# Kernel tuning notes

Measured on AMD Instinct MI355X. Metric: run time of the kernel, lower is better.

The kernel has to match this reference:

```python
import jax, jax.numpy as jnp
import numpy as np

EPS = 1e-3  # BatchNormalization epsilon


def setup_inputs() -> dict:
    key = jax.random.key(0)
    ks = jax.random.split(key, 8)
    B, H, W, C = 16, 128, 128, 128
    f = C // 2  # filters = max(1, C // 2)
    x = jax.random.normal(ks[0], (B, H, W, C), dtype=jnp.float32)
    s_in = 1.0 / np.sqrt(C)
    s_f = 1.0 / np.sqrt(f)
    return {
        "x": x,
        "Wg": jax.random.normal(ks[1], (C, f), dtype=jnp.float32) * s_in,
        "bg": jnp.zeros((f,), jnp.float32),
        "Wt": jax.random.normal(ks[2], (C, f), dtype=jnp.float32) * s_in,
        "bt": jnp.zeros((f,), jnp.float32),
        "Wp": jax.random.normal(ks[3], (C, f), dtype=jnp.float32) * s_in,
        "bp": jnp.zeros((f,), jnp.float32),
        "Wo": jax.random.normal(ks[4], (f, f), dtype=jnp.float32) * s_f,
        "bo": jnp.zeros((f,), jnp.float32),
        "gamma": jnp.ones((f,), jnp.float32),
        "beta": jnp.zeros((f,), jnp.float32),
        "moving_mean": jnp.zeros((f,), jnp.float32),
        "moving_var": jnp.ones((f,), jnp.float32),
    }


def reference(x, Wg, bg, Wt, bt, Wp, bp, Wo, bo, gamma, beta, moving_mean, moving_var):
    B, H, W, C = x.shape
    f = Wg.shape[1]
    N = H * W
    # 1x1 conv projections (NHWC): einsum over channel dim, then flatten spatial
    g = (jnp.einsum('bhwc,cf->bhwf', x, Wg) + bg).reshape(B, N, f)     # [B,N,f]
    tx = (jnp.einsum('bhwc,cf->bhwf', x, Wt) + bt).reshape(B, N, f)    # theta
    ty = (jnp.einsum('bhwc,cf->bhwf', x, Wp) + bp).reshape(B, N, f)    # phi
    # keras Dot(axes=[1,2]) on ([B,N,f], Permute->[B,f,N]) contracts the N axes
    # -> f x f Gram matrix per batch element.
    fm = jnp.einsum('bni,bnj->bij', tx, ty)                            # [B,f,f]
    fm = jax.nn.softmax(fm, axis=-1)
    # second Dot(axes=[1,2]): contract fm axis 1 (i) with g axis 2 (i) -> [B,f,N]
    z = jnp.einsum('bij,bni->bjn', fm, g)                              # [B,f,N]
    # Reshape flat-reinterprets [B, f*N] as [B,H,W,f]
    z = z.reshape(B, H, W, f)
    # output 1x1 conv (f -> f channels)
    z = jnp.einsum('bhwf,fe->bhwe', z, Wo) + bo
    # BatchNorm, inference mode (moving statistics)
    inv = gamma * jax.lax.rsqrt(moving_var + EPS)
    z = (z - moving_mean) * inv + beta
    return z
```

## Files before the change

kernel.cpp:

```cpp
#include <hip/hip_runtime.h>
#include <stdint.h>

#define B_ 16
#define H_ 128
#define W_ 128
#define C_ 128
#define F_ 64
#define N_ (H_*W_)
#define SPLITS 32
#define RPB (N_/SPLITS)
#define CH 64
#define NCH (RPB/CH)
#define EPSV 1e-3f

typedef __attribute__((ext_vector_type(8))) short bf16x8;
typedef __attribute__((ext_vector_type(16))) float f32x16;

__device__ __forceinline__ unsigned short f2b(float f) {
    unsigned int x = __float_as_uint(f);
    x += 0x7fffu + ((x >> 16) & 1u);
    return (unsigned short)(x >> 16);
}
__device__ __forceinline__ float b2f(unsigned short u) {
    return __uint_as_float(((unsigned int)u) << 16);
}

__global__ __launch_bounds__(256, 2)
void kS(const float* __restrict__ x, const float* __restrict__ Wg,
        const float* __restrict__ bg, unsigned short* __restrict__ g,
        float* __restrict__ Spart, float* __restrict__ cspart)
{
    __shared__ unsigned int  xsT_hi[C_][36];
    __shared__ unsigned int  xsT_lo[C_][36];
    __shared__ __align__(16) unsigned short xs_pool[CH][136];
    __shared__ __align__(16) unsigned short gT[CH][72];

    const int tid  = threadIdx.x;
    const int lane = tid & 63;
    const int w    = tid >> 6;
    const int b    = blockIdx.x >> 5;
    const int sp   = blockIdx.x & 31;

    const float* xb = x + ((size_t)b * N_ + (size_t)sp * RPB) * C_;
    unsigned short* gb = g + ((size_t)b * N_ + (size_t)sp * RPB) * F_;

    const int rowA = lane & 31;
    const int hiL  = lane >> 5;
    const int kgrp = hiL * 8;
    const int c1b  = (w & 1) * 64;
    const int c2b  = (w >> 1) * 64;
    const int nbG  = (w & 1) * 32;
    const int fbG  = (w >> 1) * 32;

    const float bgl = bg[fbG + rowA];

    for (int i = tid; i < C_*F_; i += 256) {
        int c = i >> 6, f = i & 63;
        xs_pool[f][c] = f2b(Wg[i]);
    }
    __syncthreads();
    bf16x8 wgfr[8];
    #pragma unroll
    for (int ks = 0; ks < 8; ++ks)
        wgfr[ks] = *(const bf16x8*)&xs_pool[fbG + rowA][ks*16 + kgrp];
    __syncthreads();

    f32x16 accS[2][2];
    #pragma unroll
    for (int ti = 0; ti < 2; ++ti)
        #pragma unroll
        for (int tj = 0; tj < 2; ++tj)
            #pragma unroll
            for (int e = 0; e < 16; ++e) accS[ti][tj][e] = 0.f;

    float4 csr[4];
    #pragma unroll
    for (int p = 0; p < 4; ++p) csr[p] = make_float4(0.f, 0.f, 0.f, 0.f);

    const int sr = tid >> 2;
    const int sc = (tid & 3) * 16;

    for (int ch = 0; ch < NCH; ++ch) {
        __syncthreads();

        float4 ra[4], rq[4];
        {
            const float* xc = xb + (size_t)ch * CH * C_;
            #pragma unroll
            for (int p = 0; p < 4; ++p) {
                const int idx = tid + 256*p;
                const float* r0 = xc + (size_t)(2*(idx & 31)) * C_ + ((idx >> 5) * 4);
                ra[p] = *(const float4*)r0;
                rq[p] = *(const float4*)(r0 + C_);
            }
        }
        uint4 gv0, gv1;
        if (ch) {
            gv0 = *(const uint4*)&gT[sr][sc];
            gv1 = *(const uint4*)&gT[sr][sc + 8];
        }

        #pragma unroll
        for (int p = 0; p < 4; ++p) {
            const int idx = tid + 256*p;
            const int np  = idx & 31;
            const int c4  = (idx >> 5) * 4;
            float4 a = ra[p], q = rq[p];
            csr[p].x += a.x + q.x;
            csr[p].y += a.y + q.y;
            csr[p].z += a.z + q.z;
            csr[p].w += a.w + q.w;
            unsigned short ha0 = f2b(a.x), ha1 = f2b(a.y), ha2 = f2b(a.z), ha3 = f2b(a.w);
            unsigned short hb0 = f2b(q.x), hb1 = f2b(q.y), hb2 = f2b(q.z), hb3 = f2b(q.w);
            unsigned short la0 = f2b(a.x - b2f(ha0)), la1 = f2b(a.y - b2f(ha1));
            unsigned short la2 = f2b(a.z - b2f(ha2)), la3 = f2b(a.w - b2f(ha3));
            unsigned short lb0 = f2b(q.x - b2f(hb0)), lb1 = f2b(q.y - b2f(hb1));
            unsigned short lb2 = f2b(q.z - b2f(hb2)), lb3 = f2b(q.w - b2f(hb3));
            xsT_hi[c4+0][np] = (unsigned)ha0 | ((unsigned)hb0 << 16);
            xsT_hi[c4+1][np] = (unsigned)ha1 | ((unsigned)hb1 << 16);
            xsT_hi[c4+2][np] = (unsigned)ha2 | ((unsigned)hb2 << 16);
            xsT_hi[c4+3][np] = (unsigned)ha3 | ((unsigned)hb3 << 16);
            xsT_lo[c4+0][np] = (unsigned)la0 | ((unsigned)lb0 << 16);
            xsT_lo[c4+1][np] = (unsigned)la1 | ((unsigned)lb1 << 16);
            xsT_lo[c4+2][np] = (unsigned)la2 | ((unsigned)lb2 << 16);
            xsT_lo[c4+3][np] = (unsigned)la3 | ((unsigned)lb3 << 16);
            ushort4 u0; u0.x = ha0; u0.y = ha1; u0.z = ha2; u0.w = ha3;
            ushort4 u1; u1.x = hb0; u1.y = hb1; u1.z = hb2; u1.w = hb3;
            *(ushort4*)&xs_pool[2*np  ][c4] = u0;
            *(ushort4*)&xs_pool[2*np+1][c4] = u1;
        }

        if (ch) {
            unsigned short* dst = gb + (size_t)((ch-1)*CH + sr) * F_ + sc;
            *(uint4*)dst       = gv0;
            *(uint4*)(dst + 8) = gv1;
        }
        __syncthreads();

        {
            f32x16 aG;
            #pragma unroll
            for (int e = 0; e < 16; ++e) aG[e] = 0.f;
            #pragma unroll
            for (int ks = 0; ks < 8; ++ks) {
                bf16x8 av = *(const bf16x8*)&xs_pool[nbG + rowA][ks*16 + kgrp];
                aG = __builtin_amdgcn_mfma_f32_32x32x16_bf16(av, wgfr[ks], aG, 0, 0, 0);
            }
            const int fcol = fbG + rowA;
            #pragma unroll
            for (int r = 0; r < 16; ++r) {
                int nloc = (r & 3) + 8*(r >> 2) + 4*hiL;
                gT[nbG + nloc][fcol] = f2b(aG[r] + bgl);
            }
        }

        #pragma unroll
        for (int ks = 0; ks < 4; ++ks) {
            const int kn = ks*16 + kgrp;
            bf16x8 Ah[2], Al[2], Bh[2], Bl[2];
            #pragma unroll
            for (int t = 0; t < 2; ++t) {
                const unsigned short* rAh = (const unsigned short*)&xsT_hi[c1b + 32*t + rowA][0];
                const unsigned short* rAl = (const unsigned short*)&xsT_lo[c1b + 32*t + rowA][0];
                Ah[t] = *(const bf16x8*)(rAh + kn);
                Al[t] = *(const bf16x8*)(rAl + kn);
                const unsigned short* rBh = (const unsigned short*)&xsT_hi[c2b + 32*t + rowA][0];
                const unsigned short* rBl = (const unsigned short*)&xsT_lo[c2b + 32*t + rowA][0];
                Bh[t] = *(const bf16x8*)(rBh + kn);
                Bl[t] = *(const bf16x8*)(rBl + kn);
            }
            #pragma unroll
            for (int ti = 0; ti < 2; ++ti)
                #pragma unroll
                for (int tj = 0; tj < 2; ++tj) {
                    accS[ti][tj] = __builtin_amdgcn_mfma_f32_32x32x16_bf16(Ah[ti], Bh[tj], accS[ti][tj], 0, 0, 0);
                    accS[ti][tj] = __builtin_amdgcn_mfma_f32_32x32x16_bf16(Ah[ti], Bl[tj], accS[ti][tj], 0, 0, 0);
                    accS[ti][tj] = __builtin_amdgcn_mfma_f32_32x32x16_bf16(Al[ti], Bh[tj], accS[ti][tj], 0, 0, 0);
                }
        }
    }

    __syncthreads();
    {
        uint4 gv0 = *(const uint4*)&gT[sr][sc];
        uint4 gv1 = *(const uint4*)&gT[sr][sc + 8];
        unsigned short* dst = gb + (size_t)((NCH - 1)*CH + sr) * F_ + sc;
        *(uint4*)dst       = gv0;
        *(uint4*)(dst + 8) = gv1;
    }

    float* so = Spart + (size_t)(b * SPLITS + sp) * (size_t)(C_ * C_);
    #pragma unroll
    for (int ti = 0; ti < 2; ++ti)
        #pragma unroll
        for (int tj = 0; tj < 2; ++tj)
            #pragma unroll
            for (int r = 0; r < 16; ++r) {
                int c1 = c1b + 32*ti + (r & 3) + 8*(r >> 2) + 4*hiL;
                int c2 = c2b + 32*tj + rowA;
                so[(size_t)c1 * C_ + c2] = accS[ti][tj][r];
            }

    #pragma unroll
    for (int p = 0; p < 4; ++p) {
        #pragma unroll
        for (int o = 16; o; o >>= 1) {
            csr[p].x += __shfl_xor(csr[p].x, o);
            csr[p].y += __shfl_xor(csr[p].y, o);
            csr[p].z += __shfl_xor(csr[p].z, o);
            csr[p].w += __shfl_xor(csr[p].w, o);
        }
    }
    if ((lane & 31) == 0) {
        const int h = lane >> 5;
        float* co = cspart + (size_t)(b * SPLITS + sp) * C_;
        #pragma unroll
        for (int p = 0; p < 4; ++p) {
            const int c4 = 4 * (2*w + h + 8*p);
            co[c4+0] = csr[p].x;
            co[c4+1] = csr[p].y;
            co[c4+2] = csr[p].z;
            co[c4+3] = csr[p].w;
        }
    }
}

__global__ __launch_bounds__(256, 8)
void kR(const float* __restrict__ Spart, const float* __restrict__ cspart,
        float* __restrict__ Sred, float* __restrict__ csred)
{
    const int b = blockIdx.x >> 4;
    const int r = blockIdx.x & 15;
    const int f4 = r*256 + threadIdx.x;
    const float4* base = (const float4*)(Spart + (size_t)b * SPLITS * C_ * C_);
    float sx=0.f, sy=0.f, sz=0.f, sw=0.f;
    #pragma unroll 4
    for (int sp = 0; sp < SPLITS; ++sp) {
        float4 v = base[(size_t)sp * (C_*C_/4) + f4];
        sx += v.x; sy += v.y; sz += v.z; sw += v.w;
    }
    ((float4*)(Sred + (size_t)b * C_ * C_))[f4] = make_float4(sx, sy, sz, sw);

    if (r == 0 && threadIdx.x < C_) {
        float c = 0.f;
        #pragma unroll 4
        for (int sp = 0; sp < SPLITS; ++sp)
            c += cspart[((size_t)b * SPLITS + sp) * C_ + threadIdx.x];
        csred[(size_t)b * C_ + threadIdx.x] = c;
    }
}

__global__ __launch_bounds__(256, 2)
void kT(const float* __restrict__ Sred, const float* __restrict__ csred,
        const float* __restrict__ Wp, float* __restrict__ T1buf,
        float* __restrict__ T2buf)
{
    __shared__ float Ss[32][C_];
    __shared__ float Wps[C_][F_];

    const int tid = threadIdx.x;
    const int b = blockIdx.x >> 2;
    const int q = blockIdx.x & 3;

    const float4* sg = (const float4*)(Sred + ((size_t)b * C_ + q*32) * C_);
    for (int t = tid; t < 32*C_/4; t += 256) ((float4*)Ss)[t] = sg[t];
    const float4* wg = (const float4*)Wp;
    for (int t = tid; t < C_*F_/4; t += 256) ((float4*)Wps)[t] = wg[t];
    __syncthreads();

    const int lane = tid & 63;
    const int w    = tid >> 6;

    float acc[8] = {0.f,0.f,0.f,0.f,0.f,0.f,0.f,0.f};
    #pragma unroll 2
    for (int k = 0; k < C_; k += 4) {
        float w0 = Wps[k+0][lane];
        float w1 = Wps[k+1][lane];
        float w2 = Wps[k+2][lane];
        float w3 = Wps[k+3][lane];
        #pragma unroll
        for (int cl = 0; cl < 8; ++cl) {
            float4 sv = *(const float4*)&Ss[w*8 + cl][k];
            float t = acc[cl];
            t = fmaf(sv.x, w0, t);
            t = fmaf(sv.y, w1, t);
            t = fmaf(sv.z, w2, t);
            t = fmaf(sv.w, w3, t);
            acc[cl] = t;
        }
    }
    #pragma unroll
    for (int cl = 0; cl < 8; ++cl) {
        int c = q*32 + w*8 + cl;
        T1buf[((size_t)b * C_ + c) * F_ + lane] = acc[cl];
    }

    if (q == 0 && tid < F_) {
        const float* cv = csred + (size_t)b * C_;
        float s = 0.f;
        for (int k = 0; k < C_; ++k) s = fmaf(cv[k], Wps[k][tid], s);
        T2buf[(size_t)b * F_ + tid] = s;
    }
}

__global__ __launch_bounds__(256, 2)
void kF(const float* __restrict__ T1buf, const float* __restrict__ T2buf,
        const float* __restrict__ csred, const float* __restrict__ Wt,
        const float* __restrict__ bt, const float* __restrict__ bp,
        float* __restrict__ U)
{
    __shared__ float T1s[C_][F_];
    __shared__ float Wts[C_][F_];
    __shared__ float csb[C_];
    __shared__ float T2s[F_], T3s[F_], bts[F_], bps[F_];

    const int tid = threadIdx.x;
    const int b = blockIdx.x;

    for (int t = tid; t < C_*F_/4; t += 256) {
        ((float4*)T1s)[t] = ((const float4*)(T1buf + (size_t)b * C_ * F_))[t];
        ((float4*)Wts)[t] = ((const float4*)Wt)[t];
    }
    if (tid < C_) csb[tid] = csred[(size_t)b * C_ + tid];
    if (tid < F_) {
        T2s[tid] = T2buf[(size_t)b * F_ + tid];
        bts[tid] = bt[tid];
        bps[tid] = bp[tid];
    }
    __syncthreads();

    if (tid < F_) {
        float s = 0.f;
        for (int c = 0; c < C_; ++c) s = fmaf(csb[c], Wts[c][tid], s);
        T3s[tid] = s;
    }
    __syncthreads();

    const int lane = tid & 63;
    const int w    = tid >> 6;

    float acc[16];
    #pragma unroll
    for (int r = 0; r < 16; ++r) acc[r] = 0.f;

    #pragma unroll 2
    for (int c = 0; c < C_; ++c) {
        float t1 = T1s[c][lane];
        #pragma unroll
        for (int u = 0; u < 4; ++u) {
            float4 wv = *(const float4*)&Wts[c][w*16 + u*4];
            acc[u*4+0] = fmaf(wv.x, t1, acc[u*4+0]);
            acc[u*4+1] = fmaf(wv.y, t1, acc[u*4+1]);
            acc[u*4+2] = fmaf(wv.z, t1, acc[u*4+2]);
            acc[u*4+3] = fmaf(wv.w, t1, acc[u*4+3]);
        }
    }

    const float bpj = bps[lane];
    const float t2j = T2s[lane];
    #pragma unroll
    for (int r = 0; r < 16; ++r) {
        const int i = w*16 + r;
        float v = acc[r] + T3s[i]*bpj + bts[i]*(t2j + (float)N_ * bpj);
        float m = v;
        #pragma unroll
        for (int o = 32; o; o >>= 1) m = fmaxf(m, __shfl_xor(m, o));
        float e = expf(v - m);
        float s = e;
        #pragma unroll
        for (int o = 32; o; o >>= 1) s += __shfl_xor(s, o);
        U[((size_t)b * F_ + i) * F_ + lane] = e / s;
    }
}

__global__ __launch_bounds__(256, 2)
void kC(const unsigned short* __restrict__ g, const float* __restrict__ U,
        const float* __restrict__ Wo, const float* __restrict__ bo,
        const float* __restrict__ gamma_, const float* __restrict__ beta_,
        const float* __restrict__ mmean, const float* __restrict__ mvar,
        float* __restrict__ out)
{
    __shared__ __align__(16) unsigned short UT[F_][72];
    __shared__ __align__(16) unsigned short WoT[F_][72];
    __shared__ __align__(16) unsigned short M1T[4][32][72];

    const int tid  = threadIdx.x;
    const int lane = tid & 63;
    const int wv   = tid >> 6;
    const int jt   = wv & 1;
    const int et   = wv >> 1;

    const int wgrp = blockIdx.x & 15;
    const int half = (blockIdx.x >> 4) & 1;
    const int b    = blockIdx.x >> 5;

    for (int t = tid; t < 1024; t += 256) {
        const int i  = t >> 4;
        const int j4 = (t & 15) * 4;
        float4 uv = *(const float4*)(U + ((size_t)b * F_ + i) * F_ + j4);
        UT[j4+0][i] = f2b(uv.x); UT[j4+1][i] = f2b(uv.y);
        UT[j4+2][i] = f2b(uv.z); UT[j4+3][i] = f2b(uv.w);
        float4 wo4 = *(const float4*)(Wo + (size_t)i * F_ + j4);
        WoT[j4+0][i] = f2b(wo4.x); WoT[j4+1][i] = f2b(wo4.y);
        WoT[j4+2][i] = f2b(wo4.z); WoT[j4+3][i] = f2b(wo4.w);
    }
    __syncthreads();

    const int rowA = lane & 31;
    const int hi   = lane >> 5;
    const int hi8  = hi * 8;

    bf16x8 Ufr[4], WoFr[4];
    #pragma unroll
    for (int ks = 0; ks < 4; ++ks) {
        Ufr[ks]  = *(const bf16x8*)&UT [32*jt + rowA][16*ks + hi8];
        WoFr[ks] = *(const bf16x8*)&WoT[32*et + rowA][16*ks + hi8];
    }

    const int ep = 32*et + rowA;
    const float scl = gamma_[ep] * rsqrtf(mvar[ep] + EPSV);
    const float sft = (bo[ep] - mmean[ep]) * scl + beta_[ep];

    const unsigned short* gB = g + ((size_t)b * N_ + (size_t)half * (N_/2)) * F_;
    float* outB = out + (((size_t)b * H_ + half) * W_) * F_ + ep;
    const int w0 = wgrp * 8;

    unsigned short* m1row = &M1T[wv][rowA][0];

    auto gload = [&](bf16x8 (&D)[2][4], int widx) {
        const unsigned short* gw = gB + (size_t)widx * (64*F_) + (size_t)rowA * F_ + hi8;
        #pragma unroll
        for (int ft = 0; ft < 2; ++ft)
            #pragma unroll
            for (int ks = 0; ks < 4; ++ks)
                D[ft][ks] = *(const bf16x8*)(gw + ft*(32*F_) + 16*ks);
    };

    auto body = [&](bf16x8 (&G)[2][4], int widx) {
        f32x16 m0, m1, a2r;
        #pragma unroll
        for (int e = 0; e < 16; ++e) { m0[e] = 0.f; m1[e] = 0.f; a2r[e] = 0.f; }
        #pragma unroll
        for (int ks = 0; ks < 4; ++ks) {
            m0 = __builtin_amdgcn_mfma_f32_32x32x16_bf16(G[0][ks], Ufr[ks], m0, 0, 0, 0);
            m1 = __builtin_amdgcn_mfma_f32_32x32x16_bf16(G[1][ks], Ufr[ks], m1, 0, 0, 0);
        }
        #pragma unroll
        for (int r = 0; r < 16; r += 2) {
            const int e0 = (r & 3) + 8*(r >> 2) + 4*hi;
            const unsigned pw0 = (unsigned)f2b(m0[r]) | ((unsigned)f2b(m0[r+1]) << 16);
            *(unsigned int*)(m1row + e0) = pw0;
            const unsigned pw1 = (unsigned)f2b(m1[r]) | ((unsigned)f2b(m1[r+1]) << 16);
            *(unsigned int*)(m1row + 32 + e0) = pw1;
        }
        __syncthreads();
        #pragma unroll
        for (int ksg = 0; ksg < 4; ++ksg) {
            bf16x8 af = *(const bf16x8*)(m1row + 16*ksg + hi8);
            a2r = __builtin_amdgcn_mfma_f32_32x32x16_bf16(af, WoFr[ksg], a2r, 0, 0, 0);
        }
        float* ow = outB + (size_t)widx * F_ + (size_t)(64*jt + 8*hi) * (W_*F_);
        #pragma unroll
        for (int r = 0; r < 16; ++r) {
            const int off2j = 2*(r & 3) + 16*(r >> 2);
            ow[(size_t)off2j * (W_*F_)] = a2r[r] * scl + sft;
        }
        __syncthreads();
    };

    bf16x8 GA[2][4], GBf[2][4];
    gload(GA, w0);
    #pragma unroll
    for (int wi = 0; wi < 8; ++wi) {
        if (wi & 1) {
            if (wi < 7) gload(GA, w0 + wi + 1);
            body(GBf, w0 + wi);
        } else {
            if (wi < 7) gload(GBf, w0 + wi + 1);
            body(GA, w0 + wi);
        }
    }
}

extern "C" void kernel_launch(void* const* d_in, const int* in_sizes, int n_in,
                              void* d_out, int out_size, void* d_ws, size_t ws_size,
                              hipStream_t stream)
{
    const float* x  = (const float*)d_in[0];
    const float* Wg = (const float*)d_in[1];
    const float* bg = (const float*)d_in[2];
    const float* Wt = (const float*)d_in[3];
    const float* bt = (const float*)d_in[4];
    const float* Wp = (const float*)d_in[5];
    const float* bp = (const float*)d_in[6];
    const float* Wo = (const float*)d_in[7];
    const float* bo = (const float*)d_in[8];
    const float* ga = (const float*)d_in[9];
    const float* be = (const float*)d_in[10];
    const float* mm = (const float*)d_in[11];
    const float* mv = (const float*)d_in[12];
    float* out = (float*)d_out;

    char* ws = (char*)d_ws;
    unsigned short* g = (unsigned short*)ws;
    size_t off = (size_t)B_ * N_ * F_ * sizeof(unsigned short);
    float* Spart = (float*)(ws + off);
    float* T1buf = (float*)(ws + off);
    off += (size_t)B_ * SPLITS * C_ * C_ * sizeof(float);
    float* cspart = (float*)(ws + off);
    off += (size_t)B_ * SPLITS * C_ * sizeof(float);
    float* U = (float*)(ws + off);
    off += (size_t)B_ * F_ * F_ * sizeof(float);
    float* Sred = (float*)(ws + off);
    off += (size_t)B_ * C_ * C_ * sizeof(float);
    float* csred = (float*)(ws + off);
    off += (size_t)B_ * C_ * sizeof(float);
    float* T2buf = (float*)(ws + off);

    kS<<<B_ * SPLITS, 256, 0, stream>>>(x, Wg, bg, g, Spart, cspart);
    kR<<<B_ * 16, 256, 0, stream>>>(Spart, cspart, Sred, csred);
    kT<<<B_ * 4, 256, 0, stream>>>(Sred, csred, Wp, T1buf, T2buf);
    kF<<<B_, 256, 0, stream>>>(T1buf, T2buf, csred, Wt, bt, bp, U);
    kC<<<B_ * 2 * (W_/8), 256, 0, stream>>>(g, U, Wo, bo, ga, be, mm, mv, out);
}
```

Before: 107.4 us.

## Prefetch next x chunk into registers and XOR-swizzle transposed LDS tiles

```diff
diff --git a/kernel.cpp b/kernel.cpp
--- a/kernel.cpp
+++ b/kernel.cpp
@@ -80,20 +80,25 @@
     const int sr = tid >> 2;
     const int sc = (tid & 3) * 16;
 
+    const int swzR = ((rowA >> 3) & 3) << 2;
+
+    float4 ra[4], rq[4];
+    auto loadChunk = [&](int ch) {
+        const float* xc = xb + (size_t)ch * CH * C_;
+        #pragma unroll
+        for (int p = 0; p < 4; ++p) {
+            const int idx = tid + 256*p;
+            const float* r0 = xc + (size_t)(2*(idx & 31)) * C_ + ((idx >> 5) * 4);
+            ra[p] = *(const float4*)r0;
+            rq[p] = *(const float4*)(r0 + C_);
+        }
+    };
+
+    loadChunk(0);
+
     for (int ch = 0; ch < NCH; ++ch) {
         __syncthreads();
 
-        float4 ra[4], rq[4];
-        {
-            const float* xc = xb + (size_t)ch * CH * C_;
-            #pragma unroll
-            for (int p = 0; p < 4; ++p) {
-                const int idx = tid + 256*p;
-                const float* r0 = xc + (size_t)(2*(idx & 31)) * C_ + ((idx >> 5) * 4);
-                ra[p] = *(const float4*)r0;
-                rq[p] = *(const float4*)(r0 + C_);
-            }
-        }
         uint4 gv0, gv1;
         if (ch) {
             gv0 = *(const uint4*)&gT[sr][sc];
@@ -105,6 +110,7 @@
             const int idx = tid + 256*p;
             const int np  = idx & 31;
             const int c4  = (idx >> 5) * 4;
+            const int npx = np ^ (((c4 >> 3) & 3) << 2);
             float4 a = ra[p], q = rq[p];
             csr[p].x += a.x + q.x;
             csr[p].y += a.y + q.y;
@@ -116,14 +122,14 @@
             unsigned short la2 = f2b(a.z - b2f(ha2)), la3 = f2b(a.w - b2f(ha3));
             unsigned short lb0 = f2b(q.x - b2f(hb0)), lb1 = f2b(q.y - b2f(hb1));
             unsigned short lb2 = f2b(q.z - b2f(hb2)), lb3 = f2b(q.w - b2f(hb3));
-            xsT_hi[c4+0][np] = (unsigned)ha0 | ((unsigned)hb0 << 16);
-            xsT_hi[c4+1][np] = (unsigned)ha1 | ((unsigned)hb1 << 16);
-            xsT_hi[c4+2][np] = (unsigned)ha2 | ((unsigned)hb2 << 16);
-            xsT_hi[c4+3][np] = (unsigned)ha3 | ((unsigned)hb3 << 16);
-            xsT_lo[c4+0][np] = (unsigned)la0 | ((unsigned)lb0 << 16);
-            xsT_lo[c4+1][np] = (unsigned)la1 | ((unsigned)lb1 << 16);
-            xsT_lo[c4+2][np] = (unsigned)la2 | ((unsigned)lb2 << 16);
-            xsT_lo[c4+3][np] = (unsigned)la3 | ((unsigned)lb3 << 16);
+            xsT_hi[c4+0][npx] = (unsigned)ha0 | ((unsigned)hb0 << 16);
+            xsT_hi[c4+1][npx] = (unsigned)ha1 | ((unsigned)hb1 << 16);
+            xsT_hi[c4+2][npx] = (unsigned)ha2 | ((unsigned)hb2 << 16);
+            xsT_hi[c4+3][npx] = (unsigned)ha3 | ((unsigned)hb3 << 16);
+            xsT_lo[c4+0][npx] = (unsigned)la0 | ((unsigned)lb0 << 16);
+            xsT_lo[c4+1][npx] = (unsigned)la1 | ((unsigned)lb1 << 16);
+            xsT_lo[c4+2][npx] = (unsigned)la2 | ((unsigned)lb2 << 16);
+            xsT_lo[c4+3][npx] = (unsigned)la3 | ((unsigned)lb3 << 16);
             ushort4 u0; u0.x = ha0; u0.y = ha1; u0.z = ha2; u0.w = ha3;
             ushort4 u1; u1.x = hb0; u1.y = hb1; u1.z = hb2; u1.w = hb3;
             *(ushort4*)&xs_pool[2*np  ][c4] = u0;
@@ -136,6 +142,8 @@
             *(uint4*)(dst + 8) = gv1;
         }
         __syncthreads();
+
+        if (ch < NCH - 1) loadChunk(ch + 1);
 
         {
             f32x16 aG;
@@ -156,18 +164,18 @@
 
         #pragma unroll
         for (int ks = 0; ks < 4; ++ks) {
-            const int kn = ks*16 + kgrp;
+            const int ro = 2 * ((8*ks + 4*hiL) ^ swzR);
             bf16x8 Ah[2], Al[2], Bh[2], Bl[2];
             #pragma unroll
             for (int t = 0; t < 2; ++t) {
                 const unsigned short* rAh = (const unsigned short*)&xsT_hi[c1b + 32*t + rowA][0];
                 const unsigned short* rAl = (const unsigned short*)&xsT_lo[c1b + 32*t + rowA][0];
-                Ah[t] = *(const bf16x8*)(rAh + kn);
-                Al[t] = *(const bf16x8*)(rAl + kn);
+                Ah[t] = *(const bf16x8*)(rAh + ro);
+                Al[t] = *(const bf16x8*)(rAl + ro);
                 const unsigned short* rBh = (const unsigned short*)&xsT_hi[c2b + 32*t + rowA][0];
                 const unsigned short* rBl = (const unsigned short*)&xsT_lo[c2b + 32*t + rowA][0];
-                Bh[t] = *(const bf16x8*)(rBh + kn);
-                Bl[t] = *(const bf16x8*)(rBl + kn);
+                Bh[t] = *(const bf16x8*)(rBh + ro);
+                Bl[t] = *(const bf16x8*)(rBl + ro);
             }
             #pragma unroll
             for (int ti = 0; ti < 2; ++ti)
```

Result: no change. 106.9 us (-0.5%).

## Split fused Gram/g-projection kernel into two kernels with doubled splits and prefetch

Applied to the files above, without the earlier changes.

```diff
diff --git a/kernel.cpp b/kernel.cpp
--- a/kernel.cpp
+++ b/kernel.cpp
@@ -7,10 +7,10 @@
 #define C_ 128
 #define F_ 64
 #define N_ (H_*W_)
-#define SPLITS 32
-#define RPB (N_/SPLITS)
+#define SPL 64
+#define RPB2 (N_/SPL)
 #define CH 64
-#define NCH (RPB/CH)
+#define NCH2 (RPB2/CH)
 #define EPSV 1e-3f
 
 typedef __attribute__((ext_vector_type(8))) short bf16x8;
@@ -25,45 +25,26 @@
     return __uint_as_float(((unsigned int)u) << 16);
 }
 
-__global__ __launch_bounds__(256, 2)
-void kS(const float* __restrict__ x, const float* __restrict__ Wg,
-        const float* __restrict__ bg, unsigned short* __restrict__ g,
-        float* __restrict__ Spart, float* __restrict__ cspart)
-{
-    __shared__ unsigned int  xsT_hi[C_][36];
-    __shared__ unsigned int  xsT_lo[C_][36];
-    __shared__ __align__(16) unsigned short xs_pool[CH][136];
-    __shared__ __align__(16) unsigned short gT[CH][72];
+__global__ __launch_bounds__(256, 4)
+void kS2(const float* __restrict__ x,
+         float* __restrict__ Spart, float* __restrict__ cspart)
+{
+    __shared__ unsigned int xsT_hi[C_][36];
+    __shared__ unsigned int xsT_lo[C_][36];
 
     const int tid  = threadIdx.x;
     const int lane = tid & 63;
     const int w    = tid >> 6;
-    const int b    = blockIdx.x >> 5;
-    const int sp   = blockIdx.x & 31;
-
-    const float* xb = x + ((size_t)b * N_ + (size_t)sp * RPB) * C_;
-    unsigned short* gb = g + ((size_t)b * N_ + (size_t)sp * RPB) * F_;
+    const int b    = blockIdx.x >> 6;
+    const int sp   = blockIdx.x & 63;
+
+    const float* xb = x + ((size_t)b * N_ + (size_t)sp * RPB2) * C_;
 
     const int rowA = lane & 31;
     const int hiL  = lane >> 5;
     const int kgrp = hiL * 8;
     const int c1b  = (w & 1) * 64;
     const int c2b  = (w >> 1) * 64;
-    const int nbG  = (w & 1) * 32;
-    const int fbG  = (w >> 1) * 32;
-
-    const float bgl = bg[fbG + rowA];
-
-    for (int i = tid; i < C_*F_; i += 256) {
-        int c = i >> 6, f = i & 63;
-        xs_pool[f][c] = f2b(Wg[i]);
-    }
-    __syncthreads();
-    bf16x8 wgfr[8];
-    #pragma unroll
-    for (int ks = 0; ks < 8; ++ks)
-        wgfr[ks] = *(const bf16x8*)&xs_pool[fbG + rowA][ks*16 + kgrp];
-    __syncthreads();
 
     f32x16 accS[2][2];
     #pragma unroll
@@ -77,28 +58,22 @@
     #pragma unroll
     for (int p = 0; p < 4; ++p) csr[p] = make_float4(0.f, 0.f, 0.f, 0.f);
 
-    const int sr = tid >> 2;
-    const int sc = (tid & 3) * 16;
-
-    for (int ch = 0; ch < NCH; ++ch) {
+    float4 ra[4], rq[4];
+    auto loadChunk = [&](int ch) {
+        const float* xc = xb + (size_t)ch * CH * C_;
+        #pragma unroll
+        for (int p = 0; p < 4; ++p) {
+            const int idx = tid + 256*p;
+            const float* r0 = xc + (size_t)(2*(idx & 31)) * C_ + ((idx >> 5) * 4);
+            ra[p] = *(const float4*)r0;
+            rq[p] = *(const float4*)(r0 + C_);
+        }
+    };
+
+    loadChunk(0);
+
+    for (int ch = 0; ch < NCH2; ++ch) {
         __syncthreads();
-
-        float4 ra[4], rq[4];
-        {
-            const float* xc = xb + (size_t)ch * CH * C_;
-            #pragma unroll
-            for (int p = 0; p < 4; ++p) {
-                const int idx = tid + 256*p;
-                const float* r0 = xc + (size_t)(2*(idx & 31)) * C_ + ((idx >> 5) * 4);
-                ra[p] = *(const float4*)r0;
-                rq[p] = *(const float4*)(r0 + C_);
-            }
-        }
-        uint4 gv0, gv1;
-        if (ch) {
-            gv0 = *(const uint4*)&gT[sr][sc];
-            gv1 = *(const uint4*)&gT[sr][sc + 8];
-        }
 
         #pragma unroll
         for (int p = 0; p < 4; ++p) {
@@ -124,35 +99,10 @@
             xsT_lo[c4+1][np] = (unsigned)la1 | ((unsigned)lb1 << 16);
             xsT_lo[c4+2][np] = (unsigned)la2 | ((unsigned)lb2 << 16);
             xsT_lo[c4+3][np] = (unsigned)la3 | ((unsigned)lb3 << 16);
-            ushort4 u0; u0.x = ha0; u0.y = ha1; u0.z = ha2; u0.w = ha3;
-            ushort4 u1; u1.x = hb0; u1.y = hb1; u1.z = hb2; u1.w = hb3;
-            *(ushort4*)&xs_pool[2*np  ][c4] = u0;
-            *(ushort4*)&xs_pool[2*np+1][c4] = u1;
-        }
-
-        if (ch) {
-            unsigned short* dst = gb + (size_t)((ch-1)*CH + sr) * F_ + sc;
-            *(uint4*)dst       = gv0;
-            *(uint4*)(dst + 8) = gv1;
         }
         __syncthreads();
 
-        {
-            f32x16 aG;
-            #pragma unroll
-            for (int e = 0; e < 16; ++e) aG[e] = 0.f;
-            #pragma unroll
-            for (int ks = 0; ks < 8; ++ks) {
-                bf16x8 av = *(const bf16x8*)&xs_pool[nbG + rowA][ks*16 + kgrp];
-                aG = __builtin_amdgcn_mfma_f32_32x32x16_bf16(av, wgfr[ks], aG, 0, 0, 0);
-            }
-            const int fcol = fbG + rowA;
-            #pragma unroll
-            for (int r = 0; r < 16; ++r) {
-                int nloc = (r & 3) + 8*(r >> 2) + 4*hiL;
-                gT[nbG + nloc][fcol] = f2b(aG[r] + bgl);
-            }
-        }
+        if (ch < NCH2 - 1) loadChunk(ch + 1);
 
         #pragma unroll
         for (int ks = 0; ks < 4; ++ks) {
@@ -180,16 +130,7 @@
         }
     }
 
-    __syncthreads();
-    {
-        uint4 gv0 = *(const uint4*)&gT[sr][sc];
-        uint4 gv1 = *(const uint4*)&gT[sr][sc + 8];
-        unsigned short* dst = gb + (size_t)((NCH - 1)*CH + sr) * F_ + sc;
-        *(uint4*)dst       = gv0;
-        *(uint4*)(dst + 8) = gv1;
-    }
-
-    float* so = Spart + (size_t)(b * SPLITS + sp) * (size_t)(C_ * C_);
+    float* so = Spart + (size_t)(b * SPL + sp) * (size_t)(C_ * C_);
     #pragma unroll
     for (int ti = 0; ti < 2; ++ti)
         #pragma unroll
@@ -213,7 +154,7 @@
     }
     if ((lane & 31) == 0) {
         const int h = lane >> 5;
-        float* co = cspart + (size_t)(b * SPLITS + sp) * C_;
+        float* co = cspart + (size_t)(b * SPL + sp) * C_;
         #pragma unroll
         for (int p = 0; p < 4; ++p) {
             const int c4 = 4 * (2*w + h + 8*p);
@@ -225,6 +166,116 @@
     }
 }
 
+__global__ __launch_bounds__(256, 4)
+void kG(const float* __restrict__ x, const float* __restrict__ Wg,
+        const float* __restrict__ bg, unsigned short* __restrict__ g)
+{
+    __shared__ __align__(16) unsigned short xs_pool[CH][136];
+    __shared__ __align__(16) unsigned short gT[CH][72];
+
+    const int tid  = threadIdx.x;
+    const int lane = tid & 63;
+    const int w    = tid >> 6;
+    const int b    = blockIdx.x >> 6;
+    const int sp   = blockIdx.x & 63;
+
+    const float* xb = x + ((size_t)b * N_ + (size_t)sp * RPB2) * C_;
+    unsigned short* gb = g + ((size_t)b * N_ + (size_t)sp * RPB2) * F_;
+
+    const int rowA = lane & 31;
+    const int hiL  = lane >> 5;
+    const int kgrp = hiL * 8;
+    const int nbG  = (w & 1) * 32;
+    const int fbG  = (w >> 1) * 32;
+
+    const float bgl = bg[fbG + rowA];
+
+    for (int i = tid; i < C_*F_; i += 256) {
+        int c = i >> 6, f = i & 63;
+        xs_pool[f][c] = f2b(Wg[i]);
+    }
+    __syncthreads();
+    bf16x8 wgfr[8];
+    #pragma unroll
+    for (int ks = 0; ks < 8; ++ks)
+        wgfr[ks] = *(const bf16x8*)&xs_pool[fbG + rowA][ks*16 + kgrp];
+    __syncthreads();
+
+    const int sr = tid >> 2;
+    const int sc = (tid & 3) * 16;
+
+    float4 ra[4], rq[4];
+    auto loadChunk = [&](int ch) {
+        const float* xc = xb + (size_t)ch * CH * C_;
+        #pragma unroll
+        for (int p = 0; p < 4; ++p) {
+            const int idx = tid + 256*p;
+            const float* r0 = xc + (size_t)(2*(idx & 31)) * C_ + ((idx >> 5) * 4);
+            ra[p] = *(const float4*)r0;
+            rq[p] = *(const float4*)(r0 + C_);
+        }
+    };
+
+    loadChunk(0);
+
+    for (int ch = 0; ch < NCH2; ++ch) {
+        __syncthreads();
+
+        uint4 gv0, gv1;
+        if (ch) {
+            gv0 = *(const uint4*)&gT[sr][sc];
+            gv1 = *(const uint4*)&gT[sr][sc + 8];
+        }
+
+        #pragma unroll
+        for (int p = 0; p < 4; ++p) {
+            const int idx = tid + 256*p;
+            const int np  = idx & 31;
+            const int c4  = (idx >> 5) * 4;
+            float4 a = ra[p], q = rq[p];
+            ushort4 u0; u0.x = f2b(a.x); u0.y = f2b(a.y); u0.z = f2b(a.z); u0.w = f2b(a.w);
+            ushort4 u1; u1.x = f2b(q.x); u1.y = f2b(q.y); u1.z = f2b(q.z); u1.w = f2b(q.w);
+            *(ushort4*)&xs_pool[2*np  ][c4] = u0;
+            *(ushort4*)&xs_pool[2*np+1][c4] = u1;
+        }
+
+        if (ch) {
+            unsigned short* dst = gb + (size_t)((ch-1)*CH + sr) * F_ + sc;
+            *(uint4*)dst       = gv0;
+            *(uint4*)(dst + 8) = gv1;
+        }
+        __syncthreads();
+
+        if (ch < NCH2 - 1) loadChunk(ch + 1);
+
+        {
+            f32x16 aG;
+            #pragma unroll
+            for (int e = 0; e < 16; ++e) aG[e] = 0.f;
+            #pragma unroll
+            for (int ks = 0; ks < 8; ++ks) {
+                bf16x8 av = *(const bf16x8*)&xs_pool[nbG + rowA][ks*16 + kgrp];
+                aG = __builtin_amdgcn_mfma_f32_32x32x16_bf16(av, wgfr[ks], aG, 0, 0, 0);
+            }
+            const int fcol = fbG + rowA;
+            #pragma unroll
+            for (int r = 0; r < 16; ++r) {
+                int nloc = (r & 3) + 8*(r >> 2) + 4*hiL;
+                gT[nbG + nloc][fcol] = f2b(aG[r] + bgl);
+            }
+        }
+    }
+
+    __syncthreads();
+    {
+        uint4 gv0 = *(const uint4*)&gT[sr][sc];
+        uint4 gv1 = *(const uint4*)&gT[sr][sc + 8];
+        unsigned short* dst = gb + (size_t)((NCH2 - 1)*CH + sr) * F_ + sc;
+        *(uint4*)dst       = gv0;
+        *(uint4*)(dst + 8) = gv1;
+    }
+}
+
 __global__ __launch_bounds__(256, 8)
 void kR(const float* __restrict__ Spart, const float* __restrict__ cspart,
         float* __restrict__ Sred, float* __restrict__ csred)
@@ -232,10 +283,10 @@
     const int b = blockIdx.x >> 4;
     const int r = blockIdx.x & 15;
     const int f4 = r*256 + threadIdx.x;
-    const float4* base = (const float4*)(Spart + (size_t)b * SPLITS * C_ * C_);
+    const float4* base = (const float4*)(Spart + (size_t)b * SPL * C_ * C_);
     float sx=0.f, sy=0.f, sz=0.f, sw=0.f;
     #pragma unroll 4
-    for (int sp = 0; sp < SPLITS; ++sp) {
+    for (int sp = 0; sp < SPL; ++sp) {
         float4 v = base[(size_t)sp * (C_*C_/4) + f4];
         sx += v.x; sy += v.y; sz += v.z; sw += v.w;
     }
@@ -244,8 +295,8 @@
     if (r == 0 && threadIdx.x < C_) {
         float c = 0.f;
         #pragma unroll 4
-        for (int sp = 0; sp < SPLITS; ++sp)
-            c += cspart[((size_t)b * SPLITS + sp) * C_ + threadIdx.x];
+        for (int sp = 0; sp < SPL; ++sp)
+            c += cspart[((size_t)b * SPL + sp) * C_ + threadIdx.x];
         csred[(size_t)b * C_ + threadIdx.x] = c;
     }
 }
@@ -453,7 +504,6 @@
             const unsigned pw1 = (unsigned)f2b(m1[r]) | ((unsigned)f2b(m1[r+1]) << 16);
             *(unsigned int*)(m1row + 32 + e0) = pw1;
         }
-        __syncthreads();
         #pragma unroll
         for (int ksg = 0; ksg < 4; ++ksg) {
             bf16x8 af = *(const bf16x8*)(m1row + 16*ksg + hi8);
@@ -465,7 +515,6 @@
             const int off2j = 2*(r & 3) + 16*(r >> 2);
             ow[(size_t)off2j * (W_*F_)] = a2r[r] * scl + sft;
         }
-        __syncthreads();
     };
 
     bf16x8 GA[2][4], GBf[2][4];
@@ -506,9 +555,9 @@
     size_t off = (size_t)B_ * N_ * F_ * sizeof(unsigned short);
     float* Spart = (float*)(ws + off);
     float* T1buf = (float*)(ws + off);
-    off += (size_t)B_ * SPLITS * C_ * C_ * sizeof(float);
+    off += (size_t)B_ * SPL * C_ * C_ * sizeof(float);
     float* cspart = (float*)(ws + off);
-    off += (size_t)B_ * SPLITS * C_ * sizeof(float);
+    off += (size_t)B_ * SPL * C_ * sizeof(float);
     float* U = (float*)(ws + off);
     off += (size_t)B_ * F_ * F_ * sizeof(float);
     float* Sred = (float*)(ws + off);
@@ -517,7 +566,8 @@
     off += (size_t)B_ * C_ * sizeof(float);
     float* T2buf = (float*)(ws + off);
 
-    kS<<<B_ * SPLITS, 256, 0, stream>>>(x, Wg, bg, g, Spart, cspart);
+    kG<<<B_ * SPL, 256, 0, stream>>>(x, Wg, bg, g);
+    kS2<<<B_ * SPL, 256, 0, stream>>>(x, Spart, cspart);
     kR<<<B_ * 16, 256, 0, stream>>>(Spart, cspart, Sred, csred);
     kT<<<B_ * 4, 256, 0, stream>>>(Sred, csred, Wp, T1buf, T2buf);
     kF<<<B_, 256, 0, stream>>>(T1buf, T2buf, csred, Wt, bt, bp, U);
```

Result: slower. 222.6 us (+107.2%).
